# Kernel tuning notes

Measured on AMD Instinct MI355X. Metric: run time of the kernel, lower is better.

The kernel has to match this reference:

```python
import jax, jax.numpy as jnp
import numpy as np


def setup_inputs() -> dict:
    key = jax.random.key(0)
    k1, k2, k3, k4 = jax.random.split(key, 4)
    B, D_e, D_o, T, H, W = 4, 128, 512, 8, 32, 32
    return {
        "memory_in": jax.random.normal(k1, (B, D_e, T, H, W), dtype=jnp.float32),
        "memory_out": jax.random.normal(k2, (B, D_o, T, H, W), dtype=jnp.float32),
        "query_in": jax.random.normal(k3, (B, D_e, H, W), dtype=jnp.float32),
        "query_out": jax.random.normal(k4, (B, D_o, H, W), dtype=jnp.float32),
    }


def reference(memory_in, memory_out, query_in, query_out):
    B, D_e, T, H, W = memory_in.shape
    D_o = memory_out.shape[1]
    N = T * H * W   # memory keys
    M = H * W       # query positions
    mi = memory_in.reshape(B, D_e, N)      # [B, D_e, N]
    qi = query_in.reshape(B, D_e, M)       # [B, D_e, M]
    # scores: [B, N, M], scaled dot-product, softmax over memory axis (N)
    scale = 1.0 / np.sqrt(D_e).astype(np.float32)
    prob = jnp.einsum('bdn,bdm->bnm', mi, qi) * scale
    prob = jax.nn.softmax(prob, axis=1)
    mo = memory_out.reshape(B, D_o, N)      # [B, D_o, N]
    memory = jnp.einsum('bdn,bnm->bdm', mo, prob).reshape(B, D_o, H, W)
    out = jnp.concatenate([memory, query_out], axis=1)  # [B, 2*D_o, H, W]
    return out, prob
```

## Files before the change

kernel.cpp:

```cpp
#include <hip/hip_runtime.h>
#include <math.h>
#include <stdint.h>

constexpr int B_  = 4;
constexpr int DE_ = 128;
constexpr int DO_ = 512;
constexpr int N_  = 8192;
constexpr int M_  = 1024;
constexpr int NCHUNK_ = 32;
constexpr int SPLITK_ = 4;
constexpr int KCHUNK_ = N_ / SPLITK_;

typedef __attribute__((ext_vector_type(8))) short bf16x8;
typedef __attribute__((ext_vector_type(8))) unsigned short u16x8;
typedef __attribute__((ext_vector_type(4))) float f32x4;

static __device__ __forceinline__ uint16_t f2bf(float f) {
    uint32_t u = __builtin_bit_cast(uint32_t, f);
    u += 0x7fffu + ((u >> 16) & 1u);
    return (uint16_t)(u >> 16);
}

__global__ __launch_bounds__(256) void k_tconv(const float* __restrict__ src,
                                               uint16_t* __restrict__ dst,
                                               int ncols) {
    const int n    = blockIdx.x * 64 + (threadIdx.x & 63);
    const int dseg = threadIdx.x >> 6;
    const int b    = blockIdx.y;
    const float* s = src + (size_t)b * DE_ * ncols + n;
    uint16_t*    d = dst + ((size_t)b * ncols + n) * DE_;
    #pragma unroll
    for (int db = 0; db < 4; ++db) {
        int d0 = db * 32 + dseg * 8;
        u16x8 o;
        #pragma unroll
        for (int q = 0; q < 8; ++q) o[q] = f2bf(s[(size_t)(d0 + q) * ncols]);
        *(u16x8*)&d[d0] = o;
    }
}

__global__ __launch_bounds__(256) void k_scores_mfma(const uint16_t* __restrict__ mit,
                                                     const uint16_t* __restrict__ qit,
                                                     float* __restrict__ S) {
    __shared__ uint16_t Asm[128 * 88];
    __shared__ uint16_t Bsm[128 * 88];
    const int m0 = blockIdx.x * 128;
    const int n0 = blockIdx.y * 128;
    const int b  = blockIdx.z;
    const int tid = threadIdx.x;

    const uint16_t* A  = mit + (size_t)b * N_ * DE_;
    const uint16_t* Bq = qit + (size_t)b * M_ * DE_;

    const int srow = tid >> 3;
    const int sseg = tid & 7;

    const int w  = tid >> 6;
    const int wn = w >> 1, wm = w & 1;
    const int l  = tid & 63;
    const int lr = l & 15;
    const int lg = l >> 4;

    f32x4 acc[4][4] = {};

    for (int k0 = 0; k0 < DE_; k0 += 64) {
        #pragma unroll
        for (int i = 0; i < 4; ++i) {
            int r = srow + i * 32;
            *(bf16x8*)&Asm[r * 88 + sseg * 8] =
                *(const bf16x8*)&A[(size_t)(n0 + r) * DE_ + k0 + sseg * 8];
            *(bf16x8*)&Bsm[r * 88 + sseg * 8] =
                *(const bf16x8*)&Bq[(size_t)(m0 + r) * DE_ + k0 + sseg * 8];
        }
        __syncthreads();
        #pragma unroll
        for (int kk = 0; kk < 64; kk += 32) {
            bf16x8 a[4], p[4];
            #pragma unroll
            for (int i = 0; i < 4; ++i)
                a[i] = *(const bf16x8*)&Asm[(wn * 64 + i * 16 + lr) * 88 + kk + lg * 8];
            #pragma unroll
            for (int j = 0; j < 4; ++j)
                p[j] = *(const bf16x8*)&Bsm[(wm * 64 + j * 16 + lr) * 88 + kk + lg * 8];
            #pragma unroll
            for (int i = 0; i < 4; ++i)
                #pragma unroll
                for (int j = 0; j < 4; ++j)
                    acc[i][j] = __builtin_amdgcn_mfma_f32_16x16x32_bf16(
                        a[i], p[j], acc[i][j], 0, 0, 0);
        }
        __syncthreads();
    }

    const float scale = 0.08838834764831845f;
    float* Sp = S + (size_t)b * N_ * M_;
    #pragma unroll
    for (int i = 0; i < 4; ++i)
        #pragma unroll
        for (int j = 0; j < 4; ++j)
            #pragma unroll
            for (int r = 0; r < 4; ++r) {
                int n = n0 + wn * 64 + i * 16 + lg * 4 + r;
                int m = m0 + wm * 64 + j * 16 + lr;
                Sp[(size_t)n * M_ + m] = acc[i][j][r] * scale;
            }
}

__global__ __launch_bounds__(256) void k_scores(const float* __restrict__ mi,
                                                const float* __restrict__ qi,
                                                float* __restrict__ S) {
    __shared__ float As[32][64];
    __shared__ float Bs[32][64];
    const int m0 = blockIdx.x * 64;
    const int n0 = blockIdx.y * 64;
    const int b  = blockIdx.z;
    const int tid = threadIdx.x;
    const int tx = tid & 15;
    const int ty = tid >> 4;

    const float* miB = mi + (size_t)b * DE_ * N_;
    const float* qiB = qi + (size_t)b * DE_ * M_;

    float acc[4][4] = {};

    for (int k0 = 0; k0 < DE_; k0 += 32) {
        #pragma unroll
        for (int t = 0; t < 8; ++t) {
            int e = tid + t * 256;
            int kk = e >> 6, nn = e & 63;
            As[kk][nn] = miB[(size_t)(k0 + kk) * N_ + n0 + nn];
            Bs[kk][nn] = qiB[(size_t)(k0 + kk) * M_ + m0 + nn];
        }
        __syncthreads();
        #pragma unroll
        for (int kk = 0; kk < 32; ++kk) {
            float a[4], p[4];
            #pragma unroll
            for (int i = 0; i < 4; ++i) a[i] = As[kk][ty * 4 + i];
            #pragma unroll
            for (int j = 0; j < 4; ++j) p[j] = Bs[kk][tx * 4 + j];
            #pragma unroll
            for (int i = 0; i < 4; ++i)
                #pragma unroll
                for (int j = 0; j < 4; ++j)
                    acc[i][j] = fmaf(a[i], p[j], acc[i][j]);
        }
        __syncthreads();
    }

    const float scale = 0.08838834764831845f;
    float* Sp = S + (size_t)b * N_ * M_;
    #pragma unroll
    for (int i = 0; i < 4; ++i) {
        float4 v = make_float4(acc[i][0] * scale, acc[i][1] * scale,
                               acc[i][2] * scale, acc[i][3] * scale);
        *(float4*)&Sp[(size_t)(n0 + ty * 4 + i) * M_ + m0 + tx * 4] = v;
    }
}

__global__ __launch_bounds__(256) void k_colstats(const float* __restrict__ S,
                                                  float* __restrict__ pmax,
                                                  float* __restrict__ psum) {
    const int m = blockIdx.x * 256 + threadIdx.x;
    const int c = blockIdx.y;
    const int b = blockIdx.z;
    const float* Sp = S + (size_t)b * N_ * M_ + (size_t)c * 256 * M_ + m;
    float mx = -INFINITY, sm = 0.f;
    for (int n = 0; n < 256; ++n) {
        float x = Sp[(size_t)n * M_];
        float mnew = fmaxf(mx, x);
        sm = sm * __expf(mx - mnew) + __expf(x - mnew);
        mx = mnew;
    }
    size_t idx = ((size_t)b * NCHUNK_ + c) * M_ + m;
    pmax[idx] = mx;
    psum[idx] = sm;
}

__global__ __launch_bounds__(256) void k_reduce(const float* __restrict__ pmax,
                                                const float* __restrict__ psum,
                                                float* __restrict__ gmax,
                                                float* __restrict__ ginv) {
    const int g = blockIdx.x * 256 + threadIdx.x;
    const int b = g >> 10;
    const int m = g & (M_ - 1);
    float pm[NCHUNK_];
    float mx = -INFINITY;
    #pragma unroll
    for (int c = 0; c < NCHUNK_; ++c) {
        pm[c] = pmax[((size_t)b * NCHUNK_ + c) * M_ + m];
        mx = fmaxf(mx, pm[c]);
    }
    float sm = 0.f;
    #pragma unroll
    for (int c = 0; c < NCHUNK_; ++c) {
        sm += psum[((size_t)b * NCHUNK_ + c) * M_ + m] * __expf(pm[c] - mx);
    }
    gmax[g] = mx;
    ginv[g] = 1.0f / sm;
}

__global__ __launch_bounds__(256) void k_normalize_t(float* __restrict__ S,
                                                     const float* __restrict__ gmax,
                                                     const float* __restrict__ ginv,
                                                     uint16_t* __restrict__ Pt) {
    __shared__ float T[64][65];
    const int m0 = blockIdx.x * 64;
    const int n0 = blockIdx.y * 64;
    const int b  = blockIdx.z;
    const int t  = threadIdx.x;
    const int c  = t & 15;
    const int rr = t >> 4;

    float4 gm = *(const float4*)&gmax[b * M_ + m0 + c * 4];
    float4 gi = *(const float4*)&ginv[b * M_ + m0 + c * 4];
    float* Sp = S + (size_t)b * N_ * M_;

    #pragma unroll
    for (int it = 0; it < 4; ++it) {
        int r = rr + it * 16;
        size_t idx = (size_t)(n0 + r) * M_ + m0 + c * 4;
        float4 v = *(float4*)&Sp[idx];
        v.x = __expf(v.x - gm.x) * gi.x;
        v.y = __expf(v.y - gm.y) * gi.y;
        v.z = __expf(v.z - gm.z) * gi.z;
        v.w = __expf(v.w - gm.w) * gi.w;
        *(float4*)&Sp[idx] = v;
        T[r][c * 4 + 0] = v.x;
        T[r][c * 4 + 1] = v.y;
        T[r][c * 4 + 2] = v.z;
        T[r][c * 4 + 3] = v.w;
    }
    __syncthreads();

    const int ml = t >> 2;
    const int ns = t & 3;
    uint16_t* PtB = Pt + ((size_t)b * M_ + m0 + ml) * N_ + n0 + ns * 16;
    u16x8 s0, s1;
    #pragma unroll
    for (int jj = 0; jj < 8; ++jj) s0[jj] = f2bf(T[ns * 16 + jj][ml]);
    #pragma unroll
    for (int jj = 0; jj < 8; ++jj) s1[jj] = f2bf(T[ns * 16 + 8 + jj][ml]);
    *(u16x8*)&PtB[0] = s0;
    *(u16x8*)&PtB[8] = s1;
}

__global__ __launch_bounds__(256) void k_moconv(const float* __restrict__ mo,
                                                uint16_t* __restrict__ mo16) {
    const size_t base = ((size_t)blockIdx.x * 256 + threadIdx.x) * 16;
    float4 v0 = *(const float4*)&mo[base + 0];
    float4 v1 = *(const float4*)&mo[base + 4];
    float4 v2 = *(const float4*)&mo[base + 8];
    float4 v3 = *(const float4*)&mo[base + 12];
    u16x8 o0, o1;
    o0[0] = f2bf(v0.x); o0[1] = f2bf(v0.y); o0[2] = f2bf(v0.z); o0[3] = f2bf(v0.w);
    o0[4] = f2bf(v1.x); o0[5] = f2bf(v1.y); o0[6] = f2bf(v1.z); o0[7] = f2bf(v1.w);
    o1[0] = f2bf(v2.x); o1[1] = f2bf(v2.y); o1[2] = f2bf(v2.z); o1[3] = f2bf(v2.w);
    o1[4] = f2bf(v3.x); o1[5] = f2bf(v3.y); o1[6] = f2bf(v3.z); o1[7] = f2bf(v3.w);
    *(u16x8*)&mo16[base + 0] = o0;
    *(u16x8*)&mo16[base + 8] = o1;
}

__global__ __launch_bounds__(256) void k_pv_mfma(const uint16_t* __restrict__ mo16,
                                                 const uint16_t* __restrict__ Pt,
                                                 float* __restrict__ part) {
    __shared__ uint16_t Asm[128 * 88];
    __shared__ uint16_t Psm[128 * 88];
    const int m0 = blockIdx.x * 128;
    const int d0 = blockIdx.y * 128;
    const int b  = blockIdx.z >> 2;
    const int sk = blockIdx.z & 3;
    const int tid = threadIdx.x;

    const uint16_t* moB = mo16 + (size_t)b * DO_ * N_;
    const uint16_t* PtB = Pt   + (size_t)b * M_  * N_;

    const int srow = tid >> 3;
    const int sseg = tid & 7;

    const int w  = tid >> 6;
    const int wd = w >> 1, wm = w & 1;
    const int l  = tid & 63;
    const int lr = l & 15;
    const int lg = l >> 4;

    f32x4 acc[4][4] = {};

    for (int n0 = sk * KCHUNK_; n0 < (sk + 1) * KCHUNK_; n0 += 64) {
        #pragma unroll
        for (int i = 0; i < 4; ++i) {
            int r = srow + i * 32;
            *(bf16x8*)&Asm[r * 88 + sseg * 8] =
                *(const bf16x8*)&moB[(size_t)(d0 + r) * N_ + n0 + sseg * 8];
            *(bf16x8*)&Psm[r * 88 + sseg * 8] =
                *(const bf16x8*)&PtB[(size_t)(m0 + r) * N_ + n0 + sseg * 8];
        }
        __syncthreads();
        #pragma unroll
        for (int kk = 0; kk < 64; kk += 32) {
            bf16x8 a[4], p[4];
            #pragma unroll
            for (int i = 0; i < 4; ++i)
                a[i] = *(const bf16x8*)&Asm[(wd * 64 + i * 16 + lr) * 88 + kk + lg * 8];
            #pragma unroll
            for (int j = 0; j < 4; ++j)
                p[j] = *(const bf16x8*)&Psm[(wm * 64 + j * 16 + lr) * 88 + kk + lg * 8];
            #pragma unroll
            for (int i = 0; i < 4; ++i)
                #pragma unroll
                for (int j = 0; j < 4; ++j)
                    acc[i][j] = __builtin_amdgcn_mfma_f32_16x16x32_bf16(
                        a[i], p[j], acc[i][j], 0, 0, 0);
        }
        __syncthreads();
    }

    float* pp = part + ((size_t)(sk * B_ + b) * DO_ + d0) * M_;
    #pragma unroll
    for (int i = 0; i < 4; ++i)
        #pragma unroll
        for (int j = 0; j < 4; ++j)
            #pragma unroll
            for (int r = 0; r < 4; ++r) {
                int d = wd * 64 + i * 16 + lg * 4 + r;
                int m = wm * 64 + j * 16 + lr;
                pp[(size_t)d * M_ + m0 + m] = acc[i][j][r];
            }
}

__global__ __launch_bounds__(256) void k_pvreduce(const float* __restrict__ part,
                                                  float* __restrict__ out) {
    constexpr size_t OUTSZ = (size_t)B_ * DO_ * M_;
    const size_t i = (size_t)blockIdx.x * 256 + threadIdx.x;
    const size_t e = i * 4;
    float4 a = *(const float4*)&part[e];
    float4 b = *(const float4*)&part[OUTSZ + e];
    float4 c = *(const float4*)&part[2 * OUTSZ + e];
    float4 d = *(const float4*)&part[3 * OUTSZ + e];
    a.x += b.x + c.x + d.x;
    a.y += b.y + c.y + d.y;
    a.z += b.z + c.z + d.z;
    a.w += b.w + c.w + d.w;
    const int bb = (int)(e / ((size_t)DO_ * M_));
    const size_t rem = e % ((size_t)DO_ * M_);
    *(float4*)&out[(size_t)bb * 2 * DO_ * M_ + rem] = a;
}

__global__ __launch_bounds__(256) void k_normalize(float* __restrict__ S,
                                                   const float* __restrict__ gmax,
                                                   const float* __restrict__ ginv) {
    const size_t total4 = (size_t)B_ * N_ * M_ / 4;
    for (size_t i = (size_t)blockIdx.x * 256 + threadIdx.x; i < total4;
         i += (size_t)gridDim.x * 256) {
        size_t e = i * 4;
        int b = (int)(e / ((size_t)N_ * M_));
        int m = (int)(e & (M_ - 1));
        float4 v = ((float4*)S)[i];
        float4 gm = *(const float4*)&gmax[b * M_ + m];
        float4 gi = *(const float4*)&ginv[b * M_ + m];
        v.x = __expf(v.x - gm.x) * gi.x;
        v.y = __expf(v.y - gm.y) * gi.y;
        v.z = __expf(v.z - gm.z) * gi.z;
        v.w = __expf(v.w - gm.w) * gi.w;
        ((float4*)S)[i] = v;
    }
}

__global__ __launch_bounds__(256) void k_pv(const float* __restrict__ mo,
                                            const float* __restrict__ P,
                                            float* __restrict__ out) {
    __shared__ float As[32][68];
    __shared__ float Ps[32][64];
    const int m0 = blockIdx.x * 64;
    const int d0 = blockIdx.y * 64;
    const int b  = blockIdx.z;
    const int tid = threadIdx.x;
    const int tx = tid & 15;
    const int ty = tid >> 4;

    const float* moB = mo + (size_t)b * DO_ * N_;
    const float* PB  = P  + (size_t)b * N_ * M_;

    float acc[4][4] = {};

    for (int n0 = 0; n0 < N_; n0 += 32) {
        #pragma unroll
        for (int t = 0; t < 8; ++t) {
            int e = tid + t * 256;
            int dd = e >> 5, nn = e & 31;
            As[nn][dd] = moB[(size_t)(d0 + dd) * N_ + n0 + nn];
        }
        #pragma unroll
        for (int t = 0; t < 8; ++t) {
            int e = tid + t * 256;
            int kk = e >> 6, mm = e & 63;
            Ps[kk][mm] = PB[(size_t)(n0 + kk) * M_ + m0 + mm];
        }
        __syncthreads();
        #pragma unroll
        for (int kk = 0; kk < 32; ++kk) {
            float a[4], p[4];
            #pragma unroll
            for (int i = 0; i < 4; ++i) a[i] = As[kk][ty * 4 + i];
            #pragma unroll
            for (int j = 0; j < 4; ++j) p[j] = Ps[kk][tx * 4 + j];
            #pragma unroll
            for (int i = 0; i < 4; ++i)
                #pragma unroll
                for (int j = 0; j < 4; ++j)
                    acc[i][j] = fmaf(a[i], p[j], acc[i][j]);
        }
        __syncthreads();
    }

    float* outB = out + (size_t)b * 2 * DO_ * M_;
    #pragma unroll
    for (int i = 0; i < 4; ++i) {
        float4 v = make_float4(acc[i][0], acc[i][1], acc[i][2], acc[i][3]);
        *(float4*)&outB[(size_t)(d0 + ty * 4 + i) * M_ + m0 + tx * 4] = v;
    }
}

__global__ __launch_bounds__(256) void k_copyq(const float* __restrict__ q,
                                               float* __restrict__ out) {
    const size_t i = (size_t)blockIdx.x * 256 + threadIdx.x;
    const size_t e = i * 4;
    const int b = (int)(e / ((size_t)DO_ * M_));
    const size_t r = e % ((size_t)DO_ * M_);
    float4 v = *(const float4*)&q[e];
    *(float4*)&out[(size_t)b * 2 * DO_ * M_ + (size_t)DO_ * M_ + r] = v;
}

extern "C" void kernel_launch(void* const* d_in, const int* in_sizes, int n_in,
                              void* d_out, int out_size, void* d_ws, size_t ws_size,
                              hipStream_t stream) {
    const float* mi = (const float*)d_in[0];
    const float* mo = (const float*)d_in[1];
    const float* qi = (const float*)d_in[2];
    const float* qo = (const float*)d_in[3];

    float* out  = (float*)d_out;
    float* prob = out + (size_t)B_ * 2 * DO_ * M_;

    float* pmax = (float*)d_ws;
    float* psum = pmax + (size_t)B_ * NCHUNK_ * M_;
    float* gmax = psum + (size_t)B_ * NCHUNK_ * M_;
    float* ginv = gmax + (size_t)B_ * M_;
    uint16_t* Pt   = (uint16_t*)(ginv + B_ * M_);
    uint16_t* mo16 = Pt + (size_t)B_ * M_ * N_;
    float*    part = (float*)(mo16 + (size_t)B_ * DO_ * N_);
    uint16_t* mit  = (uint16_t*)(part + (size_t)SPLITK_ * B_ * DO_ * M_);
    uint16_t* qit  = mit + (size_t)B_ * N_ * DE_;
    const size_t need_fast =
        (size_t)((char*)mit - (char*)d_ws);
    const size_t need_full =
        (size_t)((char*)(qit + (size_t)B_ * M_ * DE_) - (char*)d_ws);

    if (ws_size >= need_full) {
        k_tconv      <<<dim3(N_ / 64, B_), 256, 0, stream>>>(mi, mit, N_);
        k_tconv      <<<dim3(M_ / 64, B_), 256, 0, stream>>>(qi, qit, M_);
        k_scores_mfma<<<dim3(M_ / 128, N_ / 128, B_), 256, 0, stream>>>(mit, qit, prob);
    } else {
        k_scores<<<dim3(M_ / 64, N_ / 64, B_), 256, 0, stream>>>(mi, qi, prob);
    }

    k_colstats<<<dim3(M_ / 256, NCHUNK_, B_), 256, 0, stream>>>(prob, pmax, psum);
    k_reduce  <<<dim3(B_ * M_ / 256), 256, 0, stream>>>(pmax, psum, gmax, ginv);

    if (ws_size >= need_fast) {
        k_moconv     <<<dim3((B_ * DO_ * N_ / 16) / 256), 256, 0, stream>>>(mo, mo16);
        k_normalize_t<<<dim3(M_ / 64, N_ / 64, B_), 256, 0, stream>>>(prob, gmax, ginv, Pt);
        k_pv_mfma    <<<dim3(M_ / 128, DO_ / 128, B_ * SPLITK_), 256, 0, stream>>>(mo16, Pt, part);
        k_pvreduce   <<<dim3((B_ * DO_ * M_ / 4) / 256), 256, 0, stream>>>(part, out);
    } else {
        k_normalize<<<dim3(2048), 256, 0, stream>>>(prob, gmax, ginv);
        k_pv       <<<dim3(M_ / 64, DO_ / 64, B_), 256, 0, stream>>>(mo, prob, out);
    }
    k_copyq<<<dim3((B_ * DO_ * M_ / 4) / 256), 256, 0, stream>>>(qo, out);
}
```

Before: 388.6 us.

## Recompute scores to fuse softmax stats and normalization into MFMA GEMM epilogues

Replaces the write-scores / column-stats / normalize-transpose pipeline with two passes of the bf16 MFMA score GEMM. The first pass reduces per-tile column max and sum in registers and shared memory and writes only small partials. The second recomputes the scores and writes the normalized prob plus the transposed bf16 copy directly. This removes a full fp32 read and rewrite of the 128 MB score matrix at the cost of running the cheap K=128 GEMM twice. The scattered per-element stores in the epilogue may be less coalesced.

```diff
diff --git a/kernel.cpp b/kernel.cpp
--- a/kernel.cpp
+++ b/kernel.cpp
@@ -8,11 +8,13 @@
 constexpr int N_  = 8192;
 constexpr int M_  = 1024;
 constexpr int NCHUNK_ = 32;
+constexpr int NT_  = 64;
 constexpr int SPLITK_ = 4;
 constexpr int KCHUNK_ = N_ / SPLITK_;
 
 typedef __attribute__((ext_vector_type(8))) short bf16x8;
 typedef __attribute__((ext_vector_type(8))) unsigned short u16x8;
+typedef __attribute__((ext_vector_type(4))) unsigned short u16x4;
 typedef __attribute__((ext_vector_type(4))) float f32x4;
 
 static __device__ __forceinline__ uint16_t f2bf(float f) {
@@ -39,210 +41,156 @@
     }
 }
 
-__global__ __launch_bounds__(256) void k_scores_mfma(const uint16_t* __restrict__ mit,
-                                                     const uint16_t* __restrict__ qit,
-                                                     float* __restrict__ S) {
+#define SCORES_MFMA_CORE(ASMV, BSMV)                                           \
+    const int m0 = blockIdx.x * 128;                                           \
+    const int n0 = blockIdx.y * 128;                                           \
+    const int b  = blockIdx.z;                                                 \
+    const int tid = threadIdx.x;                                               \
+    const uint16_t* A  = mit + (size_t)b * N_ * DE_;                           \
+    const uint16_t* Bq = qit + (size_t)b * M_ * DE_;                           \
+    const int srow = tid >> 3;                                                 \
+    const int sseg = tid & 7;                                                  \
+    const int w  = tid >> 6;                                                   \
+    const int wn = w >> 1, wm = w & 1;                                         \
+    const int l  = tid & 63;                                                   \
+    const int lr = l & 15;                                                     \
+    const int lg = l >> 4;                                                     \
+    f32x4 acc[4][4] = {};                                                      \
+    for (int k0 = 0; k0 < DE_; k0 += 64) {                                     \
+        _Pragma("unroll")                                                      \
+        for (int i = 0; i < 4; ++i) {                                          \
+            int r = srow + i * 32;                                             \
+            *(bf16x8*)&ASMV[r * 88 + sseg * 8] =                               \
+                *(const bf16x8*)&A[(size_t)(n0 + r) * DE_ + k0 + sseg * 8];    \
+            *(bf16x8*)&BSMV[r * 88 + sseg * 8] =                               \
+                *(const bf16x8*)&Bq[(size_t)(m0 + r) * DE_ + k0 + sseg * 8];   \
+        }                                                                      \
+        __syncthreads();                                                       \
+        _Pragma("unroll")                                                      \
+        for (int kk = 0; kk < 64; kk += 32) {                                  \
+            bf16x8 a[4], p[4];                                                 \
+            _Pragma("unroll")                                                  \
+            for (int i = 0; i < 4; ++i)                                        \
+                a[i] = *(const bf16x8*)&ASMV[(wn*64 + i*16 + lr)*88 + kk + lg*8]; \
+            _Pragma("unroll")                                                  \
+            for (int j = 0; j < 4; ++j)                                        \
+                p[j] = *(const bf16x8*)&BSMV[(wm*64 + j*16 + lr)*88 + kk + lg*8]; \
+            _Pragma("unroll")                                                  \
+            for (int i = 0; i < 4; ++i)                                        \
+                _Pragma("unroll")                                              \
+                for (int j = 0; j < 4; ++j)                                    \
+                    acc[i][j] = __builtin_amdgcn_mfma_f32_16x16x32_bf16(       \
+                        a[i], p[j], acc[i][j], 0, 0, 0);                       \
+        }                                                                      \
+        __syncthreads();                                                       \
+    }
+
+__global__ __launch_bounds__(256) void k_stats_mfma(const uint16_t* __restrict__ mit,
+                                                    const uint16_t* __restrict__ qit,
+                                                    float* __restrict__ pmax2,
+                                                    float* __restrict__ psum2) {
     __shared__ uint16_t Asm[128 * 88];
     __shared__ uint16_t Bsm[128 * 88];
-    const int m0 = blockIdx.x * 128;
-    const int n0 = blockIdx.y * 128;
-    const int b  = blockIdx.z;
-    const int tid = threadIdx.x;
-
-    const uint16_t* A  = mit + (size_t)b * N_ * DE_;
-    const uint16_t* Bq = qit + (size_t)b * M_ * DE_;
-
-    const int srow = tid >> 3;
-    const int sseg = tid & 7;
-
-    const int w  = tid >> 6;
-    const int wn = w >> 1, wm = w & 1;
-    const int l  = tid & 63;
-    const int lr = l & 15;
-    const int lg = l >> 4;
-
-    f32x4 acc[4][4] = {};
-
-    for (int k0 = 0; k0 < DE_; k0 += 64) {
-        #pragma unroll
-        for (int i = 0; i < 4; ++i) {
-            int r = srow + i * 32;
-            *(bf16x8*)&Asm[r * 88 + sseg * 8] =
-                *(const bf16x8*)&A[(size_t)(n0 + r) * DE_ + k0 + sseg * 8];
-            *(bf16x8*)&Bsm[r * 88 + sseg * 8] =
-                *(const bf16x8*)&Bq[(size_t)(m0 + r) * DE_ + k0 + sseg * 8];
-        }
-        __syncthreads();
-        #pragma unroll
-        for (int kk = 0; kk < 64; kk += 32) {
-            bf16x8 a[4], p[4];
-            #pragma unroll
-            for (int i = 0; i < 4; ++i)
-                a[i] = *(const bf16x8*)&Asm[(wn * 64 + i * 16 + lr) * 88 + kk + lg * 8];
-            #pragma unroll
-            for (int j = 0; j < 4; ++j)
-                p[j] = *(const bf16x8*)&Bsm[(wm * 64 + j * 16 + lr) * 88 + kk + lg * 8];
-            #pragma unroll
-            for (int i = 0; i < 4; ++i)
-                #pragma unroll
-                for (int j = 0; j < 4; ++j)
-                    acc[i][j] = __builtin_amdgcn_mfma_f32_16x16x32_bf16(
-                        a[i], p[j], acc[i][j], 0, 0, 0);
-        }
-        __syncthreads();
-    }
+    __shared__ float wmx[2][128];
+    __shared__ float wsm[2][128];
+
+    SCORES_MFMA_CORE(Asm, Bsm)
 
     const float scale = 0.08838834764831845f;
-    float* Sp = S + (size_t)b * N_ * M_;
-    #pragma unroll
-    for (int i = 0; i < 4; ++i)
-        #pragma unroll
-        for (int j = 0; j < 4; ++j)
-            #pragma unroll
-            for (int r = 0; r < 4; ++r) {
-                int n = n0 + wn * 64 + i * 16 + lg * 4 + r;
-                int m = m0 + wm * 64 + j * 16 + lr;
-                Sp[(size_t)n * M_ + m] = acc[i][j][r] * scale;
-            }
-}
-
-__global__ __launch_bounds__(256) void k_scores(const float* __restrict__ mi,
-                                                const float* __restrict__ qi,
-                                                float* __restrict__ S) {
-    __shared__ float As[32][64];
-    __shared__ float Bs[32][64];
-    const int m0 = blockIdx.x * 64;
-    const int n0 = blockIdx.y * 64;
-    const int b  = blockIdx.z;
-    const int tid = threadIdx.x;
-    const int tx = tid & 15;
-    const int ty = tid >> 4;
-
-    const float* miB = mi + (size_t)b * DE_ * N_;
-    const float* qiB = qi + (size_t)b * DE_ * M_;
-
-    float acc[4][4] = {};
-
-    for (int k0 = 0; k0 < DE_; k0 += 32) {
-        #pragma unroll
-        for (int t = 0; t < 8; ++t) {
-            int e = tid + t * 256;
-            int kk = e >> 6, nn = e & 63;
-            As[kk][nn] = miB[(size_t)(k0 + kk) * N_ + n0 + nn];
-            Bs[kk][nn] = qiB[(size_t)(k0 + kk) * M_ + m0 + nn];
-        }
-        __syncthreads();
-        #pragma unroll
-        for (int kk = 0; kk < 32; ++kk) {
-            float a[4], p[4];
-            #pragma unroll
-            for (int i = 0; i < 4; ++i) a[i] = As[kk][ty * 4 + i];
-            #pragma unroll
-            for (int j = 0; j < 4; ++j) p[j] = Bs[kk][tx * 4 + j];
-            #pragma unroll
-            for (int i = 0; i < 4; ++i)
-                #pragma unroll
-                for (int j = 0; j < 4; ++j)
-                    acc[i][j] = fmaf(a[i], p[j], acc[i][j]);
-        }
-        __syncthreads();
-    }
-
-    const float scale = 0.08838834764831845f;
-    float* Sp = S + (size_t)b * N_ * M_;
-    #pragma unroll
-    for (int i = 0; i < 4; ++i) {
-        float4 v = make_float4(acc[i][0] * scale, acc[i][1] * scale,
-                               acc[i][2] * scale, acc[i][3] * scale);
-        *(float4*)&Sp[(size_t)(n0 + ty * 4 + i) * M_ + m0 + tx * 4] = v;
-    }
-}
-
-__global__ __launch_bounds__(256) void k_colstats(const float* __restrict__ S,
-                                                  float* __restrict__ pmax,
-                                                  float* __restrict__ psum) {
-    const int m = blockIdx.x * 256 + threadIdx.x;
-    const int c = blockIdx.y;
-    const int b = blockIdx.z;
-    const float* Sp = S + (size_t)b * N_ * M_ + (size_t)c * 256 * M_ + m;
-    float mx = -INFINITY, sm = 0.f;
-    for (int n = 0; n < 256; ++n) {
-        float x = Sp[(size_t)n * M_];
-        float mnew = fmaxf(mx, x);
-        sm = sm * __expf(mx - mnew) + __expf(x - mnew);
-        mx = mnew;
-    }
-    size_t idx = ((size_t)b * NCHUNK_ + c) * M_ + m;
-    pmax[idx] = mx;
-    psum[idx] = sm;
-}
-
-__global__ __launch_bounds__(256) void k_reduce(const float* __restrict__ pmax,
-                                                const float* __restrict__ psum,
-                                                float* __restrict__ gmax,
-                                                float* __restrict__ ginv) {
+    #pragma unroll
+    for (int j = 0; j < 4; ++j) {
+        float mx = -INFINITY;
+        #pragma unroll
+        for (int i = 0; i < 4; ++i)
+            #pragma unroll
+            for (int r = 0; r < 4; ++r)
+                mx = fmaxf(mx, acc[i][j][r] * scale);
+        mx = fmaxf(mx, __shfl_xor(mx, 16));
+        mx = fmaxf(mx, __shfl_xor(mx, 32));
+        float sm = 0.f;
+        #pragma unroll
+        for (int i = 0; i < 4; ++i)
+            #pragma unroll
+            for (int r = 0; r < 4; ++r)
+                sm += __expf(acc[i][j][r] * scale - mx);
+        sm += __shfl_xor(sm, 16);
+        sm += __shfl_xor(sm, 32);
+        if (lg == 0) {
+            int col = wm * 64 + j * 16 + lr;
+            wmx[wn][col] = mx;
+            wsm[wn][col] = sm;
+        }
+    }
+    __syncthreads();
+    if (tid < 128) {
+        float ma = wmx[0][tid], mb = wmx[1][tid];
+        float mx = fmaxf(ma, mb);
+        float sm = wsm[0][tid] * __expf(ma - mx) + wsm[1][tid] * __expf(mb - mx);
+        size_t o = ((size_t)b * NT_ + blockIdx.y) * M_ + m0 + tid;
+        pmax2[o] = mx;
+        psum2[o] = sm;
+    }
+}
+
+__global__ __launch_bounds__(256) void k_reduce2(const float* __restrict__ pmax2,
+                                                 const float* __restrict__ psum2,
+                                                 float* __restrict__ gmax,
+                                                 float* __restrict__ ginv) {
     const int g = blockIdx.x * 256 + threadIdx.x;
     const int b = g >> 10;
     const int m = g & (M_ - 1);
-    float pm[NCHUNK_];
-    float mx = -INFINITY;
-    #pragma unroll
-    for (int c = 0; c < NCHUNK_; ++c) {
-        pm[c] = pmax[((size_t)b * NCHUNK_ + c) * M_ + m];
-        mx = fmaxf(mx, pm[c]);
-    }
-    float sm = 0.f;
-    #pragma unroll
-    for (int c = 0; c < NCHUNK_; ++c) {
-        sm += psum[((size_t)b * NCHUNK_ + c) * M_ + m] * __expf(pm[c] - mx);
+    float mx = -INFINITY, sm = 0.f;
+    for (int c = 0; c < NT_; ++c) {
+        size_t idx = ((size_t)b * NT_ + c) * M_ + m;
+        float pm = pmax2[idx];
+        float ps = psum2[idx];
+        float mnew = fmaxf(mx, pm);
+        sm = sm * __expf(mx - mnew) + ps * __expf(pm - mnew);
+        mx = mnew;
     }
     gmax[g] = mx;
     ginv[g] = 1.0f / sm;
 }
 
-__global__ __launch_bounds__(256) void k_normalize_t(float* __restrict__ S,
-                                                     const float* __restrict__ gmax,
-                                                     const float* __restrict__ ginv,
-                                                     uint16_t* __restrict__ Pt) {
-    __shared__ float T[64][65];
-    const int m0 = blockIdx.x * 64;
-    const int n0 = blockIdx.y * 64;
-    const int b  = blockIdx.z;
-    const int t  = threadIdx.x;
-    const int c  = t & 15;
-    const int rr = t >> 4;
-
-    float4 gm = *(const float4*)&gmax[b * M_ + m0 + c * 4];
-    float4 gi = *(const float4*)&ginv[b * M_ + m0 + c * 4];
+__global__ __launch_bounds__(256) void k_prob_mfma(const uint16_t* __restrict__ mit,
+                                                   const uint16_t* __restrict__ qit,
+                                                   const float* __restrict__ gmax,
+                                                   const float* __restrict__ ginv,
+                                                   float* __restrict__ S,
+                                                   uint16_t* __restrict__ Pt) {
+    __shared__ uint16_t Asm[128 * 88];
+    __shared__ uint16_t Bsm[128 * 88];
+
+    SCORES_MFMA_CORE(Asm, Bsm)
+
+    const float scale = 0.08838834764831845f;
+    float gm[4], gi[4];
+    #pragma unroll
+    for (int j = 0; j < 4; ++j) {
+        int m = m0 + wm * 64 + j * 16 + lr;
+        gm[j] = gmax[b * M_ + m];
+        gi[j] = ginv[b * M_ + m];
+    }
     float* Sp = S + (size_t)b * N_ * M_;
-
-    #pragma unroll
-    for (int it = 0; it < 4; ++it) {
-        int r = rr + it * 16;
-        size_t idx = (size_t)(n0 + r) * M_ + m0 + c * 4;
-        float4 v = *(float4*)&Sp[idx];
-        v.x = __expf(v.x - gm.x) * gi.x;
-        v.y = __expf(v.y - gm.y) * gi.y;
-        v.z = __expf(v.z - gm.z) * gi.z;
-        v.w = __expf(v.w - gm.w) * gi.w;
-        *(float4*)&Sp[idx] = v;
-        T[r][c * 4 + 0] = v.x;
-        T[r][c * 4 + 1] = v.y;
-        T[r][c * 4 + 2] = v.z;
-        T[r][c * 4 + 3] = v.w;
-    }
-    __syncthreads();
-
-    const int ml = t >> 2;
-    const int ns = t & 3;
-    uint16_t* PtB = Pt + ((size_t)b * M_ + m0 + ml) * N_ + n0 + ns * 16;
-    u16x8 s0, s1;
-    #pragma unroll
-    for (int jj = 0; jj < 8; ++jj) s0[jj] = f2bf(T[ns * 16 + jj][ml]);
-    #pragma unroll
-    for (int jj = 0; jj < 8; ++jj) s1[jj] = f2bf(T[ns * 16 + 8 + jj][ml]);
-    *(u16x8*)&PtB[0] = s0;
-    *(u16x8*)&PtB[8] = s1;
+    uint16_t* Ptp = Pt + (size_t)b * M_ * N_;
+    #pragma unroll
+    for (int i = 0; i < 4; ++i)
+        #pragma unroll
+        for (int j = 0; j < 4; ++j) {
+            float p[4];
+            #pragma unroll
+            for (int r = 0; r < 4; ++r)
+                p[r] = __expf(acc[i][j][r] * scale - gm[j]) * gi[j];
+            const int n = n0 + wn * 64 + i * 16 + lg * 4;
+            const int m = m0 + wm * 64 + j * 16 + lr;
+            #pragma unroll
+            for (int r = 0; r < 4; ++r)
+                Sp[(size_t)(n + r) * M_ + m] = p[r];
+            u16x4 o;
+            #pragma unroll
+            for (int r = 0; r < 4; ++r) o[r] = f2bf(p[r]);
+            *(u16x4*)&Ptp[(size_t)m * N_ + n] = o;
+        }
 }
 
 __global__ __launch_bounds__(256) void k_moconv(const float* __restrict__ mo,
@@ -344,6 +292,100 @@
     const int bb = (int)(e / ((size_t)DO_ * M_));
     const size_t rem = e % ((size_t)DO_ * M_);
     *(float4*)&out[(size_t)bb * 2 * DO_ * M_ + rem] = a;
+}
+
+__global__ __launch_bounds__(256) void k_scores(const float* __restrict__ mi,
+                                                const float* __restrict__ qi,
+                                                float* __restrict__ S) {
+    __shared__ float As[32][64];
+    __shared__ float Bs[32][64];
+    const int m0 = blockIdx.x * 64;
+    const int n0 = blockIdx.y * 64;
+    const int b  = blockIdx.z;
+    const int tid = threadIdx.x;
+    const int tx = tid & 15;
+    const int ty = tid >> 4;
+
+    const float* miB = mi + (size_t)b * DE_ * N_;
+    const float* qiB = qi + (size_t)b * DE_ * M_;
+
+    float acc[4][4] = {};
+
+    for (int k0 = 0; k0 < DE_; k0 += 32) {
+        #pragma unroll
+        for (int t = 0; t < 8; ++t) {
+            int e = tid + t * 256;
+            int kk = e >> 6, nn = e & 63;
+            As[kk][nn] = miB[(size_t)(k0 + kk) * N_ + n0 + nn];
+            Bs[kk][nn] = qiB[(size_t)(k0 + kk) * M_ + m0 + nn];
+        }
+        __syncthreads();
+        #pragma unroll
+        for (int kk = 0; kk < 32; ++kk) {
+            float a[4], p[4];
+            #pragma unroll
+            for (int i = 0; i < 4; ++i) a[i] = As[kk][ty * 4 + i];
+            #pragma unroll
+            for (int j = 0; j < 4; ++j) p[j] = Bs[kk][tx * 4 + j];
+            #pragma unroll
+            for (int i = 0; i < 4; ++i)
+                #pragma unroll
+                for (int j = 0; j < 4; ++j)
+                    acc[i][j] = fmaf(a[i], p[j], acc[i][j]);
+        }
+        __syncthreads();
+    }
+
+    const float scale = 0.08838834764831845f;
+    float* Sp = S + (size_t)b * N_ * M_;
+    #pragma unroll
+    for (int i = 0; i < 4; ++i) {
+        float4 v = make_float4(acc[i][0] * scale, acc[i][1] * scale,
+                               acc[i][2] * scale, acc[i][3] * scale);
+        *(float4*)&Sp[(size_t)(n0 + ty * 4 + i) * M_ + m0 + tx * 4] = v;
+    }
+}
+
+__global__ __launch_bounds__(256) void k_colstats(const float* __restrict__ S,
+                                                  float* __restrict__ pmax,
+                                                  float* __restrict__ psum) {
+    const int m = blockIdx.x * 256 + threadIdx.x;
+    const int c = blockIdx.y;
+    const int b = blockIdx.z;
+    const float* Sp = S + (size_t)b * N_ * M_ + (size_t)c * 256 * M_ + m;
+    float mx = -INFINITY, sm = 0.f;
+    for (int n = 0; n < 256; ++n) {
+        float x = Sp[(size_t)n * M_];
+        float mnew = fmaxf(mx, x);
+        sm = sm * __expf(mx - mnew) + __expf(x - mnew);
+        mx = mnew;
+    }
+    size_t idx = ((size_t)b * NCHUNK_ + c) * M_ + m;
+    pmax[idx] = mx;
+    psum[idx] = sm;
+}
+
+__global__ __launch_bounds__(256) void k_reduce(const float* __restrict__ pmax,
+                                                const float* __restrict__ psum,
+                                                float* __restrict__ gmax,
+                                                float* __restrict__ ginv) {
+    const int g = blockIdx.x * 256 + threadIdx.x;
+    const int b = g >> 10;
+    const int m = g & (M_ - 1);
+    float pm[NCHUNK_];
+    float mx = -INFINITY;
+    #pragma unroll
+    for (int c = 0; c < NCHUNK_; ++c) {
+        pm[c] = pmax[((size_t)b * NCHUNK_ + c) * M_ + m];
+        mx = fmaxf(mx, pm[c]);
+    }
+    float sm = 0.f;
+    #pragma unroll
+    for (int c = 0; c < NCHUNK_; ++c) {
+        sm += psum[((size_t)b * NCHUNK_ + c) * M_ + m] * __expf(pm[c] - mx);
+    }
+    gmax[g] = mx;
+    ginv[g] = 1.0f / sm;
 }
 
 __global__ __launch_bounds__(256) void k_normalize(float* __restrict__ S,
@@ -442,38 +484,36 @@
     float* out  = (float*)d_out;
     float* prob = out + (size_t)B_ * 2 * DO_ * M_;
 
-    float* pmax = (float*)d_ws;
-    float* psum = pmax + (size_t)B_ * NCHUNK_ * M_;
-    float* gmax = psum + (size_t)B_ * NCHUNK_ * M_;
-    float* ginv = gmax + (size_t)B_ * M_;
+    float* pmax2 = (float*)d_ws;
+    float* psum2 = pmax2 + (size_t)B_ * NT_ * M_;
+    float* gmax  = psum2 + (size_t)B_ * NT_ * M_;
+    float* ginv  = gmax + (size_t)B_ * M_;
     uint16_t* Pt   = (uint16_t*)(ginv + B_ * M_);
     uint16_t* mo16 = Pt + (size_t)B_ * M_ * N_;
     float*    part = (float*)(mo16 + (size_t)B_ * DO_ * N_);
     uint16_t* mit  = (uint16_t*)(part + (size_t)SPLITK_ * B_ * DO_ * M_);
     uint16_t* qit  = mit + (size_t)B_ * N_ * DE_;
-    const size_t need_fast =
-        (size_t)((char*)mit - (char*)d_ws);
     const size_t need_full =
         (size_t)((char*)(qit + (size_t)B_ * M_ * DE_) - (char*)d_ws);
 
     if (ws_size >= need_full) {
-        k_tconv      <<<dim3(N_ / 64, B_), 256, 0, stream>>>(mi, mit, N_);
-        k_tconv      <<<dim3(M_ / 64, B_), 256, 0, stream>>>(qi, qit, M_);
-        k_scores_mfma<<<dim3(M_ / 128, N_ / 128, B_), 256, 0, stream>>>(mit, qit, prob);
+        k_tconv     <<<dim3(N_ / 64, B_), 256, 0, stream>>>(mi, mit, N_);
+        k_tconv     <<<dim3(M_ / 64, B_), 256, 0, stream>>>(qi, qit, M_);
+        k_stats_mfma<<<dim3(M_ / 128, N_ / 128, B_), 256, 0, stream>>>(mit, qit, pmax2, psum2);
+        k_reduce2   <<<dim3(B_ * M_ / 256), 256, 0, stream>>>(pmax2, psum2, gmax, ginv);
+        k_moconv    <<<dim3((B_ * DO_ * N_ / 16) / 256), 256, 0, stream>>>(mo, mo16);
+        k_prob_mfma <<<dim3(M_ / 128, N_ / 128, B_), 256, 0, stream>>>(mit, qit, gmax, ginv, prob, Pt);
+        k_pv_mfma   <<<dim3(M_ / 128, DO_ / 128, B_ * SPLITK_), 256, 0, stream>>>(mo16, Pt, part);
+        k_pvreduce  <<<dim3((B_ * DO_ * M_ / 4) / 256), 256, 0, stream>>>(part, out);
     } else {
-        k_scores<<<dim3(M_ / 64, N_ / 64, B_), 256, 0, stream>>>(mi, qi, prob);
-    }
-
-    k_colstats<<<dim3(M_ / 256, NCHUNK_, B_), 256, 0, stream>>>(prob, pmax, psum);
-    k_reduce  <<<dim3(B_ * M_ / 256), 256, 0, stream>>>(pmax, psum, gmax, ginv);
-
-    if (ws_size >= need_fast) {
-        k_moconv     <<<dim3((B_ * DO_ * N_ / 16) / 256), 256, 0, stream>>>(mo, mo16);
-        k_normalize_t<<<dim3(M_ / 64, N_ / 64, B_), 256, 0, stream>>>(prob, gmax, ginv, Pt);
-        k_pv_mfma    <<<dim3(M_ / 128, DO_ / 128, B_ * SPLITK_), 256, 0, stream>>>(mo16, Pt, part);
-        k_pvreduce   <<<dim3((B_ * DO_ * M_ / 4) / 256), 256, 0, stream>>>(part, out);
-    } else {
-        k_normalize<<<dim3(2048), 256, 0, stream>>>(prob, gmax, ginv);
+        float* pmax = pmax2;
+        float* psum = pmax + (size_t)B_ * NCHUNK_ * M_;
+        float* gm2  = psum + (size_t)B_ * NCHUNK_ * M_;
+        float* gi2  = gm2 + B_ * M_;
+        k_scores   <<<dim3(M_ / 64, N_ / 64, B_), 256, 0, stream>>>(mi, qi, prob);
+        k_colstats <<<dim3(M_ / 256, NCHUNK_, B_), 256, 0, stream>>>(prob, pmax, psum);
+        k_reduce   <<<dim3(B_ * M_ / 256), 256, 0, stream>>>(pmax, psum, gm2, gi2);
+        k_normalize<<<dim3(2048), 256, 0, stream>>>(prob, gm2, gi2);
         k_pv       <<<dim3(M_ / 64, DO_ / 64, B_), 256, 0, stream>>>(mo, prob, out);
     }
     k_copyq<<<dim3((B_ * DO_ * M_ / 4) / 256), 256, 0, stream>>>(qo, out);
```

Result: faster. 375.7 us (-3.3%).
